# Optimization experiments

Measured on AMD Instinct MI355X. Metric: run time of the kernel, lower is better.

Reference implementation:

```python
import jax, jax.numpy as jnp
from jax import lax
import numpy as np

IMG = 1024
STRIDES = (4, 8, 16, 32, 64)
FEAT_HW = (256, 128, 64, 32, 16)
ANCHOR_SCALE = 8.0          # per-level scale multiplier of stride
RATIOS = (0.5, 1.0, 2.0)
N_ANCHOR = len(RATIOS)
PRE_NMS = 6000
POST_NMS = 300
NMS_THRESH = 0.7
MIN_SIZE = 16.0
IMG_SCALE = 1.0
NEG = -1e9


def _conv(x, w, b, pad):
    y = lax.conv_general_dilated(x, w, (1, 1), [(pad, pad), (pad, pad)],
                                 dimension_numbers=("NCHW", "OIHW", "NCHW"))
    return y + b[None, :, None, None]


def _level_anchors(H, W, stride):
    # base anchors (ymin,xmin,ymax,xmax) centered at 0, one scale per level
    r = jnp.asarray(RATIOS, jnp.float32)
    hs = stride * ANCHOR_SCALE * jnp.sqrt(r)
    ws = stride * ANCHOR_SCALE * jnp.sqrt(1.0 / r)
    base = jnp.stack([-hs / 2, -ws / 2, hs / 2, ws / 2], axis=1)  # [A,4]
    ys = jnp.arange(H, dtype=jnp.float32) * stride
    xs = jnp.arange(W, dtype=jnp.float32) * stride
    gy, gx = jnp.meshgrid(ys, xs, indexing="ij")
    shift = jnp.stack([gy, gx, gy, gx], axis=-1).reshape(-1, 1, 4)   # [HW,1,4]
    return (shift + base[None, :, :]).reshape(-1, 4)                 # [HW*A,4]


def _decode(anchors, loc):
    ah = anchors[:, 2] - anchors[:, 0]
    aw = anchors[:, 3] - anchors[:, 1]
    acy = anchors[:, 0] + 0.5 * ah
    acx = anchors[:, 1] + 0.5 * aw
    dy, dx, dh, dw = loc[:, 0], loc[:, 1], loc[:, 2], loc[:, 3]
    cy = dy * ah + acy
    cx = dx * aw + acx
    h = jnp.exp(dh) * ah
    w = jnp.exp(dw) * aw
    boxes = jnp.stack([cy - 0.5 * h, cx - 0.5 * w, cy + 0.5 * h, cx + 0.5 * w], axis=1)
    return jnp.clip(boxes, 0.0, float(IMG))


def _iou_row(box, boxes):
    ty = jnp.maximum(box[0], boxes[:, 0])
    tx = jnp.maximum(box[1], boxes[:, 1])
    by = jnp.minimum(box[2], boxes[:, 2])
    bx = jnp.minimum(box[3], boxes[:, 3])
    inter = jnp.maximum(by - ty, 0.0) * jnp.maximum(bx - tx, 0.0)
    a1 = (box[2] - box[0]) * (box[3] - box[1])
    a2 = (boxes[:, 2] - boxes[:, 0]) * (boxes[:, 3] - boxes[:, 1])
    return inter / jnp.maximum(a1 + a2 - inter, 1e-9)


def _nms(boxes, scores):
    n = boxes.shape[0]
    idx_range = jnp.arange(n)

    def body(sc, _):
        i = jnp.argmax(sc)
        valid = sc[i] > NEG / 2
        iou = _iou_row(boxes[i], boxes)
        new_sc = jnp.where((iou > NMS_THRESH) | (idx_range == i), NEG, sc)
        sc = jnp.where(valid, new_sc, sc)
        return sc, (i, valid)

    _, (idx, keep) = lax.scan(body, scores, None, length=POST_NMS)
    return boxes[idx] * keep[:, None].astype(boxes.dtype)


def reference(p2, p3, p4, p5, p6, conv_w, conv_b, loc_w, loc_b, score_w, score_b):
    feats = [p2, p3, p4, p5, p6]
    locs, fgs, anchors = [], [], []
    for f, stride in zip(feats, STRIDES):
        h = jax.nn.relu(_conv(f, conv_w, conv_b, 1))
        loc = _conv(h, loc_w, loc_b, 0)        # [1,4A,H,W]
        sc = _conv(h, score_w, score_b, 0)     # [1,2A,H,W]
        H, W = loc.shape[2], loc.shape[3]
        loc = loc.transpose(0, 2, 3, 1).reshape(-1, 4)          # [HWA,4]
        sc = sc.transpose(0, 2, 3, 1).reshape(-1, 2)            # [HWA,2]
        fgs.append(jax.nn.softmax(sc, axis=-1)[:, 1])
        locs.append(loc)
        anchors.append(_level_anchors(H, W, stride))
    loc = jnp.concatenate(locs, axis=0)
    fg = jnp.concatenate(fgs, axis=0)
    anc = jnp.concatenate(anchors, axis=0)

    boxes = _decode(anc, loc)
    hh = boxes[:, 2] - boxes[:, 0]
    ww = boxes[:, 3] - boxes[:, 1]
    min_sz = MIN_SIZE * IMG_SCALE
    fg = jnp.where((hh >= min_sz) & (ww >= min_sz), fg, NEG)

    top_scores, top_idx = lax.top_k(fg, PRE_NMS)
    top_boxes = boxes[top_idx]
    rois = _nms(top_boxes, top_scores)   # [POST_NMS,4]
    return rois


def setup_inputs() -> dict:
    key = jax.random.key(0)
    ks = jax.random.split(key, 11)
    inp = {}
    for i, (name, hw) in enumerate(zip(["p2", "p3", "p4", "p5", "p6"], FEAT_HW)):
        inp[name] = jax.random.normal(ks[i], (1, 256, hw, hw), jnp.float32)
    inp["conv_w"] = 0.01 * jax.random.normal(ks[5], (256, 256, 3, 3), jnp.float32)
    inp["conv_b"] = jnp.zeros((256,), jnp.float32)
    inp["loc_w"] = 0.01 * jax.random.normal(ks[6], (12, 256, 1, 1), jnp.float32)
    inp["loc_b"] = jnp.zeros((12,), jnp.float32)
    inp["score_w"] = 0.01 * jax.random.normal(ks[7], (6, 256, 1, 1), jnp.float32)
    inp["score_b"] = jnp.zeros((6,), jnp.float32)
    return inp
```

## Files before the change

### kernel.cpp

```cpp
#include <hip/hip_runtime.h>
#include <hip/hip_bf16.h>

typedef unsigned int u32;
typedef unsigned long long u64;
typedef float v2f __attribute__((ext_vector_type(2)));

#define NEGV (-1000000000.0f)
#define N_ANCH 261888
#define PRE_NMS 6000
#define POST_NMS 300


__device__ __forceinline__ void gload_lds16(const float* g, float* l) {
    __builtin_amdgcn_global_load_lds((const __attribute__((address_space(1))) void*)g,
                                     (__attribute__((address_space(3))) void*)l, 16, 0, 0);
}

__device__ __forceinline__ int bucket_of(float s) {
    if (!(s > 0.0f)) return 0;
    float t = s * 4096.0f;
    int b = (int)t;
    return b > 4095 ? 4095 : b;
}

__global__ void kzero(u32* p) {
    for (int i = threadIdx.x; i < 4104; i += 1024) p[i] = 0u;
}

__global__ void wtrans(const float* __restrict__ cw, float* __restrict__ wt) {
    int g = blockIdx.x * 256 + threadIdx.x;
    int oc = g & 255; int cf = g >> 8;
    wt[g] = cw[oc * 2304 + cf];
}

__global__ __launch_bounds__(256, 4) void conv_head(
    const float* __restrict__ p2, const float* __restrict__ p3,
    const float* __restrict__ p4, const float* __restrict__ p5,
    const float* __restrict__ p6,
    const float* __restrict__ wt, const float* __restrict__ cb,
    const float* __restrict__ lw, const float* __restrict__ lb,
    const float* __restrict__ sw, const float* __restrict__ sb,
    float* __restrict__ scores_all, float4* __restrict__ boxes_all)
{
    __shared__ float smem[9696];
    float* Wl = smem;
    float* Il = smem + 9216;
    const int tid  = threadIdx.x;
    const int wv   = tid >> 6;
    const int lane = tid & 63;

    int bid = blockIdx.x;
    const float* in; int W, lg, stride, abase, local;
    if (bid < 1024)      { in = p2; W = 256; lg = 5; stride = 4;  abase = 0;      local = bid; }
    else if (bid < 1280) { in = p3; W = 128; lg = 4; stride = 8;  abase = 196608; local = bid - 1024; }
    else if (bid < 1344) { in = p4; W = 64;  lg = 3; stride = 16; abase = 245760; local = bid - 1280; }
    else if (bid < 1360) { in = p5; W = 32;  lg = 2; stride = 32; abase = 258048; local = bid - 1344; }
    else                 { in = p6; W = 16;  lg = 1; stride = 64; abase = 261120; local = bid - 1360; }
    const int bx = local & ((1 << lg) - 1), by = local >> lg;
    const int gx0 = bx * 8, gy0 = by * 8;
    const int HW = W * W;

    v2f acc2[8][4];
#pragma unroll
    for (int i = 0; i < 8; ++i)
#pragma unroll
        for (int j = 0; j < 4; ++j) acc2[i][j] = (v2f){0.0f, 0.0f};

    const int e1 = lane + 64;
    const int r0 = lane / 10, c0 = lane - r0 * 10;
    const int r1 = e1 / 10,   c1 = e1 - r1 * 10;
    const int y0g = gy0 - 1 + r0, x0g = gx0 - 1 + c0;
    const int y1g = gy0 - 1 + r1, x1g = gx0 - 1 + c1;
    const bool in0 = (y0g >= 0 && y0g < W && x0g >= 0 && x0g < W);
    const bool in1 = (lane < 36) && (y1g >= 0 && y1g < W && x1g >= 0 && x1g < W);
    const int iofs0 = y0g * W + x0g;
    const int iofs1 = y1g * W + x1g;

    for (int c = 0; c < 64; ++c) {
        __syncthreads();
        const float* gsrc = wt + c * 9216 + wv * 256 + lane * 4;
        float* ldst = Wl + wv * 256;
#pragma unroll
        for (int k = 0; k < 9; ++k)
            gload_lds16(gsrc + k * 1024, ldst + k * 1024);
        const float* ibase = in + (size_t)(c * 4 + wv) * HW;
        float v0 = in0 ? ibase[iofs0] : 0.0f;
        Il[wv * 120 + r0 * 12 + c0] = v0;
        if (lane < 36) {
            float v1 = in1 ? ibase[iofs1] : 0.0f;
            Il[wv * 120 + r1 * 12 + c1] = v1;
        }
        __syncthreads();
#pragma unroll
        for (int ic = 0; ic < 4; ++ic) {
            float wk[9];
#pragma unroll
            for (int k = 0; k < 9; ++k) wk[k] = Wl[(ic * 9 + k) * 256 + tid];
#pragma unroll
            for (int iy = 0; iy < 10; ++iy) {
                const float* rb = &Il[ic * 120 + iy * 12];
                float4 ra = *(const float4*)rb;
                float4 rbq = *(const float4*)(rb + 4);
                float2 rc = *(const float2*)(rb + 8);
                float r[10] = {ra.x, ra.y, ra.z, ra.w, rbq.x, rbq.y, rbq.z, rbq.w, rc.x, rc.y};
#pragma unroll
                for (int dy = 0; dy < 3; ++dy) {
                    const int ty = iy - dy;
                    if (ty >= 0 && ty < 8) {
                        const float w0 = wk[dy * 3 + 0], w1 = wk[dy * 3 + 1], w2 = wk[dy * 3 + 2];
#pragma unroll
                        for (int t = 0; t < 4; ++t) {
                            acc2[ty][t] = __builtin_elementwise_fma((v2f){w0, w0}, (v2f){r[2*t+0], r[2*t+1]}, acc2[ty][t]);
                            acc2[ty][t] = __builtin_elementwise_fma((v2f){w1, w1}, (v2f){r[2*t+1], r[2*t+2]}, acc2[ty][t]);
                            acc2[ty][t] = __builtin_elementwise_fma((v2f){w2, w2}, (v2f){r[2*t+2], r[2*t+3]}, acc2[ty][t]);
                        }
                    }
                }
            }
        }
    }
    {
        float bvv = cb[tid];
#pragma unroll
        for (int i = 0; i < 8; ++i)
#pragma unroll
            for (int j = 0; j < 4; ++j) {
                v2f t = acc2[i][j];
                t.x = fmaxf(t.x + bvv, 0.0f);
                t.y = fmaxf(t.y + bvv, 0.0f);
                acc2[i][j] = t;
            }
    }
    __syncthreads();
    float* hl = smem;
    float* w1 = smem + 4160;
    float* ob = smem + 8840;
    float* b1 = smem + 9160;
#pragma unroll
    for (int j = 0; j < 18; ++j) {
        int e = tid + j * 256;
        int o = e >> 8; int ch = e & 255;
        w1[o * 260 + ch] = (o < 12) ? lw[o * 256 + ch] : sw[(o - 12) * 256 + ch];
    }
    if (tid < 18) b1[tid] = (tid < 12) ? lb[tid] : sb[tid - 12];

    for (int g = 0; g < 4; ++g) {
        __syncthreads();
#pragma unroll
        for (int p = 0; p < 16; ++p) {
            const int ty = (g << 1) + (p >> 3), tx = p & 7;
            hl[p * 260 + tid] = acc2[ty][tx >> 1][tx & 1];
        }
        __syncthreads();
        for (int it = tid; it < 288; it += 256) {
            int px = it / 18, o = it - px * 18;
            float a = b1[o];
            const float4* hv4 = (const float4*)&hl[px * 260];
            const float4* wv4 = (const float4*)&w1[o * 260];
#pragma unroll 8
            for (int cc = 0; cc < 64; ++cc) {
                float4 hv = hv4[cc], wq = wv4[cc];
                a += hv.x * wq.x; a += hv.y * wq.y; a += hv.z * wq.z; a += hv.w * wq.w;
            }
            ob[px * 20 + o] = a;
        }
        __syncthreads();
        if (tid < 48) {
            int px = tid / 3, a = tid - px * 3;
            int gy = gy0 + (g << 1) + (px >> 3);
            int gx = gx0 + (px & 7);
            float dy = ob[px * 20 + a * 4 + 0];
            float dx = ob[px * 20 + a * 4 + 1];
            float dh = ob[px * 20 + a * 4 + 2];
            float dw = ob[px * 20 + a * 4 + 3];
            float s0 = ob[px * 20 + 12 + a * 2];
            float s1 = ob[px * 20 + 13 + a * 2];
            float mm = fmaxf(s0, s1);
            float e0 = expf(s0 - mm), e1x = expf(s1 - mm);
            float fg = e1x / (e0 + e1x);
            float sqa = (a == 0) ? 0.70710678f : ((a == 1) ? 1.0f : 1.41421356f);
            float sqb = (a == 0) ? 1.41421356f : ((a == 1) ? 1.0f : 0.70710678f);
            float s8 = (float)(stride * 8);
            float hs = __fmul_rn(s8, sqa), wsz = __fmul_rn(s8, sqb);
            float g_y = (float)(gy * stride), g_x = (float)(gx * stride);
            float a_y1 = __fsub_rn(g_y, __fmul_rn(hs, 0.5f));
            float a_y2 = __fadd_rn(g_y, __fmul_rn(hs, 0.5f));
            float a_x1 = __fsub_rn(g_x, __fmul_rn(wsz, 0.5f));
            float a_x2 = __fadd_rn(g_x, __fmul_rn(wsz, 0.5f));
            float ah = __fsub_rn(a_y2, a_y1), aw = __fsub_rn(a_x2, a_x1);
            float acy = __fadd_rn(a_y1, __fmul_rn(0.5f, ah));
            float acx = __fadd_rn(a_x1, __fmul_rn(0.5f, aw));
            float cy = __fadd_rn(__fmul_rn(dy, ah), acy);
            float cx = __fadd_rn(__fmul_rn(dx, aw), acx);
            float bh = __fmul_rn(expf(dh), ah);
            float bw = __fmul_rn(expf(dw), aw);
            float y1 = __fsub_rn(cy, __fmul_rn(0.5f, bh));
            float x1 = __fsub_rn(cx, __fmul_rn(0.5f, bw));
            float y2 = __fadd_rn(cy, __fmul_rn(0.5f, bh));
            float x2 = __fadd_rn(cx, __fmul_rn(0.5f, bw));
            y1 = fminf(fmaxf(y1, 0.0f), 1024.0f); x1 = fminf(fmaxf(x1, 0.0f), 1024.0f);
            y2 = fminf(fmaxf(y2, 0.0f), 1024.0f); x2 = fminf(fmaxf(x2, 0.0f), 1024.0f);
            float hh2 = __fsub_rn(y2, y1), ww2 = __fsub_rn(x2, x1);
            float sc = (hh2 >= 16.0f && ww2 >= 16.0f) ? fg : NEGV;
            int A = abase + (gy * W + gx) * 3 + a;
            scores_all[A] = sc;
            boxes_all[A] = make_float4(y1, x1, y2, x2);
        }
    }
}

__global__ void hist_k(const float* __restrict__ scores, u32* __restrict__ hist) {
    __shared__ u32 h[4096];
    int tid = threadIdx.x;
    for (int i = tid; i < 4096; i += 256) h[i] = 0u;
    __syncthreads();
    int gid = blockIdx.x * 256 + tid;
    int gs = gridDim.x * 256;
    for (int i = gid; i < N_ANCH; i += gs)
        atomicAdd(&h[bucket_of(scores[i])], 1u);
    __syncthreads();
    for (int i = tid; i < 4096; i += 256) if (h[i]) atomicAdd(&hist[i], h[i]);
}

__global__ void select_bucket(const u32* __restrict__ hist, u32* __restrict__ cnts) {
    int lane = threadIdx.x;
    u32 S = 0;
    for (int c = 0; c < 64; ++c) {
        int bin = 4095 - (c * 64 + lane);
        u32 cnt = hist[bin];
        u32 cum = cnt;
        for (int off = 1; off < 64; off <<= 1) {
            u32 n = __shfl_up(cum, off, 64);
            if (lane >= off) cum += n;
        }
        u64 ball = __ballot(S + cum >= (u32)PRE_NMS);
        if (ball) {
            int l = __ffsll((long long)ball) - 1;
            if (lane == 0) cnts[2] = (u32)(4095 - (c * 64 + l));
            return;
        }
        S += __shfl(cum, 63, 64);
    }
    if (lane == 0) cnts[2] = 0u;
}

__global__ void compact_k(const float* __restrict__ scores, u32* __restrict__ cnts,
                          u64* __restrict__ cand) {
    int B = (int)cnts[2];
    int gid = blockIdx.x * blockDim.x + threadIdx.x;
    int gs = gridDim.x * blockDim.x;
    for (int i = gid; i < N_ANCH; i += gs) {
        float s = scores[i];
        if (bucket_of(s) >= B) {
            u32 pos = atomicAdd(&cnts[0], 1u);
            if (pos < 8192u) {
                u32 u = __float_as_uint(s);
                u32 key = (u & 0x80000000u) ? ~u : (u | 0x80000000u);
                cand[pos] = ((u64)key << 32) | (u64)((u32)(~i));
            }
        }
    }
}

__global__ __launch_bounds__(1024) void sort_gather(
    const u64* __restrict__ cand, const u32* __restrict__ cnts,
    const float* __restrict__ sall, const float4* __restrict__ ball,
    float* __restrict__ nsc, float4* __restrict__ nbx, u32* __restrict__ nvalid)
{
    __shared__ u64 srt[8192];
    int tid = threadIdx.x;
    u32 total = cnts[0]; if (total > 8192u) total = 8192u;
    for (int i = tid; i < 8192; i += 1024) srt[i] = (i < (int)total) ? cand[i] : 0ULL;
    __syncthreads();
    for (int k = 2; k <= 8192; k <<= 1) {
        for (int j = k >> 1; j > 0; j >>= 1) {
            for (int i = tid; i < 8192; i += 1024) {
                int l = i ^ j;
                if (l > i) {
                    u64 a = srt[i], b = srt[l];
                    bool descRegion = (i & k) == 0;
                    if (descRegion ? (a < b) : (a > b)) { srt[i] = b; srt[l] = a; }
                }
            }
            __syncthreads();
        }
    }
    int local = 0;
    for (int i = tid; i < PRE_NMS; i += 1024) {
        u64 comp = srt[i];
        u32 idx = ~((u32)(comp & 0xFFFFFFFFULL));
        float s; float4 bx;
        if (idx < (u32)N_ANCH) { s = sall[idx]; bx = ball[idx]; }
        else { s = NEGV; bx = make_float4(0.f, 0.f, 0.f, 0.f); }
        nsc[i] = s;
        nbx[i] = bx;
        if (s > -5.0e8f) local++;
    }
    for (int off = 32; off > 0; off >>= 1) local += __shfl_down(local, off, 64);
    if ((tid & 63) == 0) atomicAdd(nvalid, (u32)local);
}

__global__ void ioumat(const float4* __restrict__ bxs, u64* __restrict__ mat) {
    int i = blockIdx.x;
    int w = threadIdx.x;
    if (w >= 94) return;
    float4 bi = bxs[i];
    float a1 = (bi.z - bi.x) * (bi.w - bi.y);
    u64 bits = 0ULL;
    int j0 = w * 64;
    for (int b = 0; b < 64; ++b) {
        int j = j0 + b;
        if (j < PRE_NMS) {
            float4 bj = bxs[j];
            float ty = fmaxf(bi.x, bj.x), tx = fmaxf(bi.y, bj.y);
            float by = fminf(bi.z, bj.z), bx = fminf(bi.w, bj.w);
            float inter = fmaxf(by - ty, 0.0f) * fmaxf(bx - tx, 0.0f);
            float a2 = (bj.z - bj.x) * (bj.w - bj.y);
            float iou = inter / fmaxf(a1 + a2 - inter, 1e-9f);
            if (iou > 0.7f) bits |= (1ULL << b);
        }
    }
    mat[(size_t)i * 94 + w] = bits;
}

__global__ void greedy(const u64* __restrict__ mat, const float* __restrict__ nbxf,
                       const u32* __restrict__ nvalid, float* __restrict__ out) {
    int lane = threadIdx.x;
    u64 rem0 = 0ULL, rem1 = 0ULL;
    int nv = (int)*nvalid; if (nv > PRE_NMS) nv = PRE_NMS;
    int kept = 0;
    for (int widx = 0; widx * 64 < nv && kept < POST_NMS; ++widx) {
        u64 word = (widx < 64) ? __shfl(rem0, widx, 64) : __shfl(rem1, widx - 64, 64);
        int bmax = nv - widx * 64; if (bmax > 64) bmax = 64;
        for (int b = 0; b < bmax; ++b) {
            if (!((word >> b) & 1ULL)) {
                int i = widx * 64 + b;
                const u64* row = mat + (size_t)i * 94;
                rem0 |= row[lane];
                if (lane < 30) rem1 |= row[64 + lane];
                if (lane < 4) out[kept * 4 + lane] = nbxf[i * 4 + lane];
                ++kept;
                if (kept == POST_NMS) break;
                word = (widx < 64) ? __shfl(rem0, widx, 64) : __shfl(rem1, widx - 64, 64);
            }
        }
        if (kept == POST_NMS) break;
    }
    for (int idx = kept * 4 + lane; idx < POST_NMS * 4; idx += 64) out[idx] = 0.0f;
}

extern "C" void kernel_launch(void* const* d_in, const int* in_sizes, int n_in,
                              void* d_out, int out_size, void* d_ws, size_t ws_size,
                              hipStream_t stream) {
    const float* p2 = (const float*)d_in[0];
    const float* p3 = (const float*)d_in[1];
    const float* p4 = (const float*)d_in[2];
    const float* p5 = (const float*)d_in[3];
    const float* p6 = (const float*)d_in[4];
    const float* cw = (const float*)d_in[5];
    const float* cb = (const float*)d_in[6];
    const float* lw = (const float*)d_in[7];
    const float* lb = (const float*)d_in[8];
    const float* sw = (const float*)d_in[9];
    const float* sb = (const float*)d_in[10];
    float* out = (float*)d_out;
    char* ws = (char*)d_ws;

    float*  scores_all = (float*)(ws + 0);
    float4* boxes_all  = (float4*)(ws + 0x100000);
    u32*    hist       = (u32*)(ws + 0x500000);
    u32*    cnts       = (u32*)(ws + 0x504000);
    u64*    cand       = (u64*)(ws + 0x505000);
    float*  nsc        = (float*)(ws + 0x520000);
    float4* nbx        = (float4*)(ws + 0x526000);
    u64*    mat        = (u64*)(ws + 0x540000);
    float*  wt         = (float*)(ws + 0x540000);

    hipLaunchKernelGGL(kzero, dim3(1), dim3(1024), 0, stream, hist);
    hipLaunchKernelGGL(wtrans, dim3(2304), dim3(256), 0, stream, cw, wt);
    hipLaunchKernelGGL(conv_head, dim3(1364), dim3(256), 0, stream,
                       p2, p3, p4, p5, p6, wt, cb, lw, lb, sw, sb,
                       scores_all, boxes_all);
    hipLaunchKernelGGL(hist_k, dim3(64), dim3(256), 0, stream, scores_all, hist);
    hipLaunchKernelGGL(select_bucket, dim3(1), dim3(64), 0, stream, hist, cnts);
    hipLaunchKernelGGL(compact_k, dim3(512), dim3(256), 0, stream, scores_all, cnts, cand);
    hipLaunchKernelGGL(sort_gather, dim3(1), dim3(1024), 0, stream,
                       cand, cnts, scores_all, boxes_all, nsc, nbx, cnts + 1);
    hipLaunchKernelGGL(ioumat, dim3(PRE_NMS), dim3(128), 0, stream, nbx, mat);
    hipLaunchKernelGGL(greedy, dim3(1), dim3(64), 0, stream, mat, (const float*)nbx, cnts + 1, out);
}
```

Before: 1.999 ms.

## Halve conv_head spatial tile to 8x4 and raise occupancy with smaller LDS

Shrinks each conv block's output tile from 8x8 to 8x4 pixels, doubling the grid to 2728 blocks. The channel loop now stages 2 input channels per step instead of 4, which cuts the accumulator count in half and reduces LDS to about 26 KB. Launch bounds rise from 4 to 6 blocks per SIMD for better latency hiding. The 1x1 head weights are now read straight from global memory rather than staged in LDS. In exchange, each weight byte is reused across fewer pixels, so global and LDS weight traffic per output doubles, and the loop needs twice as many barriers.

```diff
diff --git a/kernel.cpp b/kernel.cpp
--- a/kernel.cpp
+++ b/kernel.cpp
@@ -33,7 +33,7 @@
     wt[g] = cw[oc * 2304 + cf];
 }
 
-__global__ __launch_bounds__(256, 4) void conv_head(
+__global__ __launch_bounds__(256, 6) void conv_head(
     const float* __restrict__ p2, const float* __restrict__ p3,
     const float* __restrict__ p4, const float* __restrict__ p5,
     const float* __restrict__ p6,
@@ -42,77 +42,72 @@
     const float* __restrict__ sw, const float* __restrict__ sb,
     float* __restrict__ scores_all, float4* __restrict__ boxes_all)
 {
-    __shared__ float smem[9696];
+    __shared__ float smem[6656];
     float* Wl = smem;
-    float* Il = smem + 9216;
+    float* Il = smem + 4608;
     const int tid  = threadIdx.x;
     const int wv   = tid >> 6;
     const int lane = tid & 63;
 
     int bid = blockIdx.x;
-    const float* in; int W, lg, stride, abase, local;
-    if (bid < 1024)      { in = p2; W = 256; lg = 5; stride = 4;  abase = 0;      local = bid; }
-    else if (bid < 1280) { in = p3; W = 128; lg = 4; stride = 8;  abase = 196608; local = bid - 1024; }
-    else if (bid < 1344) { in = p4; W = 64;  lg = 3; stride = 16; abase = 245760; local = bid - 1280; }
-    else if (bid < 1360) { in = p5; W = 32;  lg = 2; stride = 32; abase = 258048; local = bid - 1344; }
-    else                 { in = p6; W = 16;  lg = 1; stride = 64; abase = 261120; local = bid - 1360; }
-    const int bx = local & ((1 << lg) - 1), by = local >> lg;
-    const int gx0 = bx * 8, gy0 = by * 8;
+    const float* in; int W, stride, abase, local, lgx;
+    if (bid < 2048)      { in = p2; W = 256; stride = 4;  abase = 0;      local = bid;        lgx = 6; }
+    else if (bid < 2560) { in = p3; W = 128; stride = 8;  abase = 196608; local = bid - 2048; lgx = 5; }
+    else if (bid < 2688) { in = p4; W = 64;  stride = 16; abase = 245760; local = bid - 2560; lgx = 4; }
+    else if (bid < 2720) { in = p5; W = 32;  stride = 32; abase = 258048; local = bid - 2688; lgx = 3; }
+    else                 { in = p6; W = 16;  stride = 64; abase = 261120; local = bid - 2720; lgx = 2; }
+    const int bx = local & ((1 << lgx) - 1), by = local >> lgx;
+    const int gx0 = bx * 4, gy0 = by * 8;
     const int HW = W * W;
 
-    v2f acc2[8][4];
+    v2f acc2[8][2];
 #pragma unroll
     for (int i = 0; i < 8; ++i)
 #pragma unroll
-        for (int j = 0; j < 4; ++j) acc2[i][j] = (v2f){0.0f, 0.0f};
-
-    const int e1 = lane + 64;
-    const int r0 = lane / 10, c0 = lane - r0 * 10;
-    const int r1 = e1 / 10,   c1 = e1 - r1 * 10;
-    const int y0g = gy0 - 1 + r0, x0g = gx0 - 1 + c0;
-    const int y1g = gy0 - 1 + r1, x1g = gx0 - 1 + c1;
-    const bool in0 = (y0g >= 0 && y0g < W && x0g >= 0 && x0g < W);
-    const bool in1 = (lane < 36) && (y1g >= 0 && y1g < W && x1g >= 0 && x1g < W);
-    const int iofs0 = y0g * W + x0g;
-    const int iofs1 = y1g * W + x1g;
-
-    for (int c = 0; c < 64; ++c) {
-        __syncthreads();
-        const float* gsrc = wt + c * 9216 + wv * 256 + lane * 4;
-        float* ldst = Wl + wv * 256;
-#pragma unroll
-        for (int k = 0; k < 9; ++k)
-            gload_lds16(gsrc + k * 1024, ldst + k * 1024);
-        const float* ibase = in + (size_t)(c * 4 + wv) * HW;
-        float v0 = in0 ? ibase[iofs0] : 0.0f;
-        Il[wv * 120 + r0 * 12 + c0] = v0;
-        if (lane < 36) {
-            float v1 = in1 ? ibase[iofs1] : 0.0f;
-            Il[wv * 120 + r1 * 12 + c1] = v1;
-        }
-        __syncthreads();
-#pragma unroll
-        for (int ic = 0; ic < 4; ++ic) {
+        for (int j = 0; j < 2; ++j) acc2[i][j] = (v2f){0.0f, 0.0f};
+
+    const int icw = wv & 1, hw_ = wv >> 1;
+    const int e = hw_ * 30 + lane;
+    const int r0 = e / 6, c0 = e - r0 * 6;
+    const int yg = gy0 - 1 + r0, xg = gx0 - 1 + c0;
+    const bool act = (lane < 30);
+    const bool inb = act && (yg >= 0 && yg < W && xg >= 0 && xg < W);
+    const int iofs = yg * W + xg;
+
+    for (int c = 0; c < 128; ++c) {
+        __syncthreads();
+        const float* gsrc = wt + c * 4608 + lane * 4;
+#pragma unroll
+        for (int k = 0; k < 5; ++k) {
+            int row = wv + k * 4;
+            if (row < 18) gload_lds16(gsrc + row * 256, Wl + row * 256);
+        }
+        const float* ibase = in + (size_t)(c * 2 + icw) * HW;
+        if (act) {
+            float v = inb ? ibase[iofs] : 0.0f;
+            Il[icw * 80 + r0 * 8 + c0] = v;
+        }
+        __syncthreads();
+#pragma unroll
+        for (int ic = 0; ic < 2; ++ic) {
             float wk[9];
 #pragma unroll
             for (int k = 0; k < 9; ++k) wk[k] = Wl[(ic * 9 + k) * 256 + tid];
 #pragma unroll
             for (int iy = 0; iy < 10; ++iy) {
-                const float* rb = &Il[ic * 120 + iy * 12];
-                float4 ra = *(const float4*)rb;
-                float4 rbq = *(const float4*)(rb + 4);
-                float2 rc = *(const float2*)(rb + 8);
-                float r[10] = {ra.x, ra.y, ra.z, ra.w, rbq.x, rbq.y, rbq.z, rbq.w, rc.x, rc.y};
+                float4 ra = *(const float4*)&Il[ic * 80 + iy * 8];
+                float2 rc = *(const float2*)&Il[ic * 80 + iy * 8 + 4];
+                float r6[6] = {ra.x, ra.y, ra.z, ra.w, rc.x, rc.y};
 #pragma unroll
                 for (int dy = 0; dy < 3; ++dy) {
                     const int ty = iy - dy;
                     if (ty >= 0 && ty < 8) {
                         const float w0 = wk[dy * 3 + 0], w1 = wk[dy * 3 + 1], w2 = wk[dy * 3 + 2];
 #pragma unroll
-                        for (int t = 0; t < 4; ++t) {
-                            acc2[ty][t] = __builtin_elementwise_fma((v2f){w0, w0}, (v2f){r[2*t+0], r[2*t+1]}, acc2[ty][t]);
-                            acc2[ty][t] = __builtin_elementwise_fma((v2f){w1, w1}, (v2f){r[2*t+1], r[2*t+2]}, acc2[ty][t]);
-                            acc2[ty][t] = __builtin_elementwise_fma((v2f){w2, w2}, (v2f){r[2*t+2], r[2*t+3]}, acc2[ty][t]);
+                        for (int t = 0; t < 2; ++t) {
+                            acc2[ty][t] = __builtin_elementwise_fma((v2f){w0, w0}, (v2f){r6[2*t+0], r6[2*t+1]}, acc2[ty][t]);
+                            acc2[ty][t] = __builtin_elementwise_fma((v2f){w1, w1}, (v2f){r6[2*t+1], r6[2*t+2]}, acc2[ty][t]);
+                            acc2[ty][t] = __builtin_elementwise_fma((v2f){w2, w2}, (v2f){r6[2*t+2], r6[2*t+3]}, acc2[ty][t]);
                         }
                     }
                 }
@@ -124,7 +119,7 @@
 #pragma unroll
         for (int i = 0; i < 8; ++i)
 #pragma unroll
-            for (int j = 0; j < 4; ++j) {
+            for (int j = 0; j < 2; ++j) {
                 v2f t = acc2[i][j];
                 t.x = fmaxf(t.x + bvv, 0.0f);
                 t.y = fmaxf(t.y + bvv, 0.0f);
@@ -133,30 +128,22 @@
     }
     __syncthreads();
     float* hl = smem;
-    float* w1 = smem + 4160;
-    float* ob = smem + 8840;
-    float* b1 = smem + 9160;
-#pragma unroll
-    for (int j = 0; j < 18; ++j) {
-        int e = tid + j * 256;
-        int o = e >> 8; int ch = e & 255;
-        w1[o * 260 + ch] = (o < 12) ? lw[o * 256 + ch] : sw[(o - 12) * 256 + ch];
-    }
-    if (tid < 18) b1[tid] = (tid < 12) ? lb[tid] : sb[tid - 12];
-
-    for (int g = 0; g < 4; ++g) {
+    float* ob = smem + 4160;
+
+    for (int g = 0; g < 2; ++g) {
         __syncthreads();
 #pragma unroll
         for (int p = 0; p < 16; ++p) {
-            const int ty = (g << 1) + (p >> 3), tx = p & 7;
+            const int ty = (g << 2) + (p >> 2), tx = p & 3;
             hl[p * 260 + tid] = acc2[ty][tx >> 1][tx & 1];
         }
         __syncthreads();
         for (int it = tid; it < 288; it += 256) {
             int px = it / 18, o = it - px * 18;
-            float a = b1[o];
+            float a = (o < 12) ? lb[o] : sb[o - 12];
+            const float* wrow = (o < 12) ? (lw + o * 256) : (sw + (o - 12) * 256);
             const float4* hv4 = (const float4*)&hl[px * 260];
-            const float4* wv4 = (const float4*)&w1[o * 260];
+            const float4* wv4 = (const float4*)wrow;
 #pragma unroll 8
             for (int cc = 0; cc < 64; ++cc) {
                 float4 hv = hv4[cc], wq = wv4[cc];
@@ -167,8 +154,8 @@
         __syncthreads();
         if (tid < 48) {
             int px = tid / 3, a = tid - px * 3;
-            int gy = gy0 + (g << 1) + (px >> 3);
-            int gx = gx0 + (px & 7);
+            int gy = gy0 + (g << 2) + (px >> 2);
+            int gx = gx0 + (px & 3);
             float dy = ob[px * 20 + a * 4 + 0];
             float dx = ob[px * 20 + a * 4 + 1];
             float dh = ob[px * 20 + a * 4 + 2];
@@ -378,7 +365,7 @@
 
     hipLaunchKernelGGL(kzero, dim3(1), dim3(1024), 0, stream, hist);
     hipLaunchKernelGGL(wtrans, dim3(2304), dim3(256), 0, stream, cw, wt);
-    hipLaunchKernelGGL(conv_head, dim3(1364), dim3(256), 0, stream,
+    hipLaunchKernelGGL(conv_head, dim3(2728), dim3(256), 0, stream,
                        p2, p3, p4, p5, p6, wt, cb, lw, lb, sw, sb,
                        scores_all, boxes_all);
     hipLaunchKernelGGL(hist_k, dim3(64), dim3(256), 0, stream, scores_all, hist);
```

New measurement: 1.999 ms. Within noise of the previous version (+0.0%).
